# Kernel optimization log

Hardware: AMD Instinct MI355X
Metric: run time of the kernel (lower is better)

The kernel has to match this reference:

```python
import jax, jax.numpy as jnp
import numpy as np

B = 512    # batch of signals
N = 1024   # time samples per signal
M = 16384  # frequency grid points (super-resolved)


def setup_inputs() -> dict:
    key = jax.random.key(0)
    x = jax.random.normal(key, (B, 2, N), dtype=jnp.float32)  # [B, 2(re/im), N]
    xgrid = jnp.linspace(-0.5, 0.5, M, dtype=jnp.float32)      # normalized freqs
    return {"x": x, "xgrid": xgrid}


def reference(x, xgrid):
    # x: [B, 2, N] -> complex signal a + i*b
    # Periodogram at arbitrary freqs f: P(f) = |sum_n x_n * exp(-2j*pi*f*n)|^2 / N
    a = x[:, 0]  # real part [B, N]
    b = x[:, 1]  # imag part [B, N]
    Nn = x.shape[-1]
    n = jnp.arange(Nn, dtype=x.dtype)
    phase = (2.0 * jnp.pi) * xgrid[:, None] * n[None, :]  # [M, N]
    C = jnp.cos(phase)  # [M, N]
    S = jnp.sin(phase)  # [M, N]
    # x_n * (cos - i sin) = (a c + b s) + i (b c - a s)
    re = jnp.einsum('bn,mn->bm', a, C) + jnp.einsum('bn,mn->bm', b, S)
    im = jnp.einsum('bn,mn->bm', b, C) - jnp.einsum('bn,mn->bm', a, S)
    return (re * re + im * im) / Nn  # [B, M]
```

## Files before the change

kernel.cpp:

```cpp
#include <hip/hip_runtime.h>


typedef __fp16 half8  __attribute__((ext_vector_type(8)));
typedef __fp16 half2v __attribute__((ext_vector_type(2)));
typedef float  f32x4  __attribute__((ext_vector_type(4)));

#define B_SZ 512
#define N_SZ 1024
#define M_SZ 16384
#define BT 128
#define MT 128
#define KT 32

union U2 { half2v h2[2]; uint2 u; };
union BF { half2v h2[4]; half8 v; uint4 u; };

__global__ __launch_bounds__(256, 2)
void periodogram_kernel(const float* __restrict__ x, const float* __restrict__ xgrid,
                        float* __restrict__ out) {
    __shared__ __align__(16) unsigned char smem[2 * 8192];
    const int tid  = (int)threadIdx.x;
    const int lane = tid & 63;
    const int w    = tid >> 6;
    const int bid  = (int)blockIdx.x;
    const int b0 = (bid & 3) * BT;
    const int m0 = (bid >> 2) * MT;

    const int wr = (w >> 1) * 64;
    const int wc = (w & 1) * 64;

    const int row8 = tid >> 3;
    const int kk   = (tid & 7) * 4;
    const int g    = kk >> 3;
    const int kkh  = (kk >> 2) & 1;

    unsigned woff[4];
    const float* srcA[4];
#pragma unroll
    for (int rep = 0; rep < 4; ++rep) {
        const int row = row8 + rep * 32;
        const int rb = row >> 4, r16 = row & 15;
        woff[rep] = (unsigned)(rb * 1024 + ((g * 16 + (r16 ^ (g << 1))) << 4) + kkh * 8);
        srcA[rep] = x + (size_t)(b0 + row) * 2048 + kk;
    }

    half2v PC[4][4], PS[4][4];
    float c0v[4], s0v[4], C32[4], S32[4];
    const float g8f = (float)((lane >> 4) << 3);
#pragma unroll
    for (int fn = 0; fn < 4; ++fn) {
        const float xg = xgrid[m0 + wc + fn * 16 + (lane & 15)];
        float Cj[8], Sj[8];
        Cj[0] = 1.0f; Sj[0] = 0.0f;
#pragma unroll
        for (int j = 1; j < 8; ++j) {
            float p = xg * (float)j; p -= floorf(p);
            Cj[j] = __builtin_amdgcn_cosf(p);
            Sj[j] = __builtin_amdgcn_sinf(p);
        }
#pragma unroll
        for (int i = 0; i < 4; ++i) {
            PC[fn][i] = __builtin_amdgcn_cvt_pkrtz(Cj[2 * i], Cj[2 * i + 1]);
            PS[fn][i] = __builtin_amdgcn_cvt_pkrtz(Sj[2 * i], Sj[2 * i + 1]);
        }
        float p32 = xg * 32.0f; p32 -= floorf(p32);
        C32[fn] = __builtin_amdgcn_cosf(p32);
        S32[fn] = __builtin_amdgcn_sinf(p32);
        float pb = xg * g8f; pb -= floorf(pb);
        c0v[fn] = __builtin_amdgcn_cosf(pb);
        s0v[fn] = __builtin_amdgcn_sinf(pb);
    }

    f32x4 accRe[4][4], accIm[4][4];
#pragma unroll
    for (int i = 0; i < 4; ++i)
#pragma unroll
        for (int j = 0; j < 4; ++j) { accRe[i][j] = (f32x4)0.0f; accIm[i][j] = (f32x4)0.0f; }

    const unsigned roff  = (unsigned)((lane ^ ((lane >> 4) << 1)) << 4);
    const unsigned aBase = 0u    + ((unsigned)(wr >> 4) << 10) + roff;
    const unsigned bBase = 8192u + ((unsigned)(wr >> 4) << 10) + roff;

    for (int t = 0; t < N_SZ / KT; ++t) {
        const int k0 = t * KT;
        float4 va[4], vb[4];
#pragma unroll
        for (int rep = 0; rep < 4; ++rep) {
            va[rep] = *(const float4*)(srcA[rep] + k0);
            vb[rep] = *(const float4*)(srcA[rep] + k0 + 1024);
        }
        __syncthreads();
#pragma unroll
        for (int rep = 0; rep < 4; ++rep) {
            U2 pa, pb;
            pa.h2[0] = __builtin_amdgcn_cvt_pkrtz(va[rep].x, va[rep].y);
            pa.h2[1] = __builtin_amdgcn_cvt_pkrtz(va[rep].z, va[rep].w);
            pb.h2[0] = __builtin_amdgcn_cvt_pkrtz(vb[rep].x, vb[rep].y);
            pb.h2[1] = __builtin_amdgcn_cvt_pkrtz(vb[rep].z, vb[rep].w);
            *(uint2*)(smem + 0    + woff[rep]) = pa.u;
            *(uint2*)(smem + 8192 + woff[rep]) = pb.u;
        }
        __syncthreads();
        half8 fa[4], fb[4];
#pragma unroll
        for (int fm = 0; fm < 4; ++fm) {
            fa[fm] = *(const half8*)(smem + aBase + fm * 1024);
            fb[fm] = *(const half8*)(smem + bBase + fm * 1024);
        }
#pragma unroll
        for (int fn = 0; fn < 4; ++fn) {
            const float c0 = c0v[fn], s0 = s0v[fn];
            const half2v c0b = __builtin_amdgcn_cvt_pkrtz(c0, c0);
            const half2v s0b = __builtin_amdgcn_cvt_pkrtz(s0, s0);
            BF fc, fs, fns;
#pragma unroll
            for (int i = 0; i < 4; ++i) {
                fc.h2[i] = c0b * PC[fn][i] - s0b * PS[fn][i];
                fs.h2[i] = s0b * PC[fn][i] + c0b * PS[fn][i];
            }
            fns.u.x = fs.u.x ^ 0x80008000u;
            fns.u.y = fs.u.y ^ 0x80008000u;
            fns.u.z = fs.u.z ^ 0x80008000u;
            fns.u.w = fs.u.w ^ 0x80008000u;
#pragma unroll
            for (int fm = 0; fm < 4; ++fm) {
                accRe[fm][fn] = __builtin_amdgcn_mfma_f32_16x16x32_f16(fa[fm], fc.v,  accRe[fm][fn], 0, 0, 0);
                accRe[fm][fn] = __builtin_amdgcn_mfma_f32_16x16x32_f16(fb[fm], fs.v,  accRe[fm][fn], 0, 0, 0);
                accIm[fm][fn] = __builtin_amdgcn_mfma_f32_16x16x32_f16(fb[fm], fc.v,  accIm[fm][fn], 0, 0, 0);
                accIm[fm][fn] = __builtin_amdgcn_mfma_f32_16x16x32_f16(fa[fm], fns.v, accIm[fm][fn], 0, 0, 0);
            }
            c0v[fn] = __builtin_fmaf(c0, C32[fn], -(s0 * S32[fn]));
            s0v[fn] = __builtin_fmaf(s0, C32[fn],  (c0 * S32[fn]));
        }
    }

    const float inv = 1.0f / (float)N_SZ;
    const int orow0 = b0 + wr + ((lane >> 4) << 2);
    const int ocol0 = m0 + wc + (lane & 15);
#pragma unroll
    for (int fm = 0; fm < 4; ++fm)
#pragma unroll
        for (int fn = 0; fn < 4; ++fn) {
            const f32x4 r = accRe[fm][fn];
            const f32x4 im = accIm[fm][fn];
            const int col = ocol0 + fn * 16;
#pragma unroll
            for (int j = 0; j < 4; ++j) {
                const int row = orow0 + fm * 16 + j;
                out[(size_t)row * M_SZ + col] = (r[j] * r[j] + im[j] * im[j]) * inv;
            }
        }
}

extern "C" void kernel_launch(void* const* d_in, const int* in_sizes, int n_in,
                              void* d_out, int out_size, void* d_ws, size_t ws_size,
                              hipStream_t stream) {
    const float* x     = (const float*)d_in[0];
    const float* xgrid = (const float*)d_in[1];
    float* out = (float*)d_out;
    dim3 grid(B_SZ / BT * (M_SZ / MT));
    dim3 block(256);
    periodogram_kernel<<<grid, block, 0, stream>>>(x, xgrid, out);
}
```

Before: 68.93 us.

## Use Gauss three-multiply complex product to cut MFMA count per tile

Replaces the four real matrix products per complex multiply with three: a·c, b·s and (a+b)·(c−s). Real and imaginary parts are then rebuilt in the epilogue as P1+P2 and P3−P1+P2. The aim is to remove a quarter of the MFMA work. In exchange it needs a third shared-memory buffer for a+b, an extra LDS read stream, a third set of accumulators (more register pressure), and accepts some fp16 precision risk from the summed operands.

```diff
diff --git a/kernel.cpp b/kernel.cpp
--- a/kernel.cpp
+++ b/kernel.cpp
@@ -18,7 +18,7 @@
 __global__ __launch_bounds__(256, 2)
 void periodogram_kernel(const float* __restrict__ x, const float* __restrict__ xgrid,
                         float* __restrict__ out) {
-    __shared__ __align__(16) unsigned char smem[2 * 8192];
+    __shared__ __align__(16) unsigned char smem[3 * 8192];
     const int tid  = (int)threadIdx.x;
     const int lane = tid & 63;
     const int w    = tid >> 6;
@@ -71,15 +71,18 @@
         s0v[fn] = __builtin_amdgcn_sinf(pb);
     }
 
-    f32x4 accRe[4][4], accIm[4][4];
+    f32x4 accP1[4][4], accP2[4][4], accP3[4][4];
 #pragma unroll
     for (int i = 0; i < 4; ++i)
 #pragma unroll
-        for (int j = 0; j < 4; ++j) { accRe[i][j] = (f32x4)0.0f; accIm[i][j] = (f32x4)0.0f; }
+        for (int j = 0; j < 4; ++j) {
+            accP1[i][j] = (f32x4)0.0f; accP2[i][j] = (f32x4)0.0f; accP3[i][j] = (f32x4)0.0f;
+        }
 
     const unsigned roff  = (unsigned)((lane ^ ((lane >> 4) << 1)) << 4);
-    const unsigned aBase = 0u    + ((unsigned)(wr >> 4) << 10) + roff;
-    const unsigned bBase = 8192u + ((unsigned)(wr >> 4) << 10) + roff;
+    const unsigned aBase = 0u     + ((unsigned)(wr >> 4) << 10) + roff;
+    const unsigned bBase = 8192u  + ((unsigned)(wr >> 4) << 10) + roff;
+    const unsigned pBase = 16384u + ((unsigned)(wr >> 4) << 10) + roff;
 
     for (int t = 0; t < N_SZ / KT; ++t) {
         const int k0 = t * KT;
@@ -92,42 +95,42 @@
         __syncthreads();
 #pragma unroll
         for (int rep = 0; rep < 4; ++rep) {
-            U2 pa, pb;
+            U2 pa, pb, pp;
             pa.h2[0] = __builtin_amdgcn_cvt_pkrtz(va[rep].x, va[rep].y);
             pa.h2[1] = __builtin_amdgcn_cvt_pkrtz(va[rep].z, va[rep].w);
             pb.h2[0] = __builtin_amdgcn_cvt_pkrtz(vb[rep].x, vb[rep].y);
             pb.h2[1] = __builtin_amdgcn_cvt_pkrtz(vb[rep].z, vb[rep].w);
-            *(uint2*)(smem + 0    + woff[rep]) = pa.u;
-            *(uint2*)(smem + 8192 + woff[rep]) = pb.u;
+            pp.h2[0] = __builtin_amdgcn_cvt_pkrtz(va[rep].x + vb[rep].x, va[rep].y + vb[rep].y);
+            pp.h2[1] = __builtin_amdgcn_cvt_pkrtz(va[rep].z + vb[rep].z, va[rep].w + vb[rep].w);
+            *(uint2*)(smem + 0     + woff[rep]) = pa.u;
+            *(uint2*)(smem + 8192  + woff[rep]) = pb.u;
+            *(uint2*)(smem + 16384 + woff[rep]) = pp.u;
         }
         __syncthreads();
-        half8 fa[4], fb[4];
+        half8 fa[4], fb[4], fp[4];
 #pragma unroll
         for (int fm = 0; fm < 4; ++fm) {
             fa[fm] = *(const half8*)(smem + aBase + fm * 1024);
             fb[fm] = *(const half8*)(smem + bBase + fm * 1024);
+            fp[fm] = *(const half8*)(smem + pBase + fm * 1024);
         }
 #pragma unroll
         for (int fn = 0; fn < 4; ++fn) {
             const float c0 = c0v[fn], s0 = s0v[fn];
             const half2v c0b = __builtin_amdgcn_cvt_pkrtz(c0, c0);
             const half2v s0b = __builtin_amdgcn_cvt_pkrtz(s0, s0);
-            BF fc, fs, fns;
+            BF fc, fs, fd;
 #pragma unroll
             for (int i = 0; i < 4; ++i) {
                 fc.h2[i] = c0b * PC[fn][i] - s0b * PS[fn][i];
                 fs.h2[i] = s0b * PC[fn][i] + c0b * PS[fn][i];
+                fd.h2[i] = fc.h2[i] - fs.h2[i];
             }
-            fns.u.x = fs.u.x ^ 0x80008000u;
-            fns.u.y = fs.u.y ^ 0x80008000u;
-            fns.u.z = fs.u.z ^ 0x80008000u;
-            fns.u.w = fs.u.w ^ 0x80008000u;
 #pragma unroll
             for (int fm = 0; fm < 4; ++fm) {
-                accRe[fm][fn] = __builtin_amdgcn_mfma_f32_16x16x32_f16(fa[fm], fc.v,  accRe[fm][fn], 0, 0, 0);
-                accRe[fm][fn] = __builtin_amdgcn_mfma_f32_16x16x32_f16(fb[fm], fs.v,  accRe[fm][fn], 0, 0, 0);
-                accIm[fm][fn] = __builtin_amdgcn_mfma_f32_16x16x32_f16(fb[fm], fc.v,  accIm[fm][fn], 0, 0, 0);
-                accIm[fm][fn] = __builtin_amdgcn_mfma_f32_16x16x32_f16(fa[fm], fns.v, accIm[fm][fn], 0, 0, 0);
+                accP1[fm][fn] = __builtin_amdgcn_mfma_f32_16x16x32_f16(fa[fm], fc.v, accP1[fm][fn], 0, 0, 0);
+                accP2[fm][fn] = __builtin_amdgcn_mfma_f32_16x16x32_f16(fb[fm], fs.v, accP2[fm][fn], 0, 0, 0);
+                accP3[fm][fn] = __builtin_amdgcn_mfma_f32_16x16x32_f16(fp[fm], fd.v, accP3[fm][fn], 0, 0, 0);
             }
             c0v[fn] = __builtin_fmaf(c0, C32[fn], -(s0 * S32[fn]));
             s0v[fn] = __builtin_fmaf(s0, C32[fn],  (c0 * S32[fn]));
@@ -141,13 +144,16 @@
     for (int fm = 0; fm < 4; ++fm)
 #pragma unroll
         for (int fn = 0; fn < 4; ++fn) {
-            const f32x4 r = accRe[fm][fn];
-            const f32x4 im = accIm[fm][fn];
+            const f32x4 p1 = accP1[fm][fn];
+            const f32x4 p2 = accP2[fm][fn];
+            const f32x4 p3 = accP3[fm][fn];
             const int col = ocol0 + fn * 16;
 #pragma unroll
             for (int j = 0; j < 4; ++j) {
+                const float re = p1[j] + p2[j];
+                const float im = p3[j] - p1[j] + p2[j];
                 const int row = orow0 + fm * 16 + j;
-                out[(size_t)row * M_SZ + col] = (r[j] * r[j] + im[j] * im[j]) * inv;
+                out[(size_t)row * M_SZ + col] = (re * re + im * im) * inv;
             }
         }
 }
```

Measured after the change: 202.6 us. 194% more time.

## Retile to 64x256 block with K=64 and all warps sharing signal rows

Applied to the files above, without the earlier changes.

Changes the block tile from 128x128 to 64 batch rows by 256 frequencies and doubles the K step to 64, processed as two 32-wide sub-steps per barrier pair. All four waves now share the same A/B fragments and each owns a distinct 64-column frequency slice. This halves the number of sync pairs per K and cuts redundant signal loads, since the cos/sin operand is generated in registers rather than loaded. In exchange, each block does more twiddle generation per frequency column and more redundant signal loads across blocks.

```diff
diff --git a/kernel.cpp b/kernel.cpp
--- a/kernel.cpp
+++ b/kernel.cpp
@@ -8,9 +8,9 @@
 #define B_SZ 512
 #define N_SZ 1024
 #define M_SZ 16384
-#define BT 128
-#define MT 128
-#define KT 32
+#define BT 64
+#define MT 256
+#define KT 64
 
 union U2 { half2v h2[2]; uint2 u; };
 union BF { half2v h2[4]; half8 v; uint4 u; };
@@ -23,25 +23,27 @@
     const int lane = tid & 63;
     const int w    = tid >> 6;
     const int bid  = (int)blockIdx.x;
-    const int b0 = (bid & 3) * BT;
-    const int m0 = (bid >> 2) * MT;
+    const int b0 = (bid & 7) * BT;
+    const int m0 = (bid >> 3) * MT;
 
-    const int wr = (w >> 1) * 64;
-    const int wc = (w & 1) * 64;
+    const int wc = w * 64;
 
     const int row8 = tid >> 3;
     const int kk   = (tid & 7) * 4;
     const int g    = kk >> 3;
     const int kkh  = (kk >> 2) & 1;
 
-    unsigned woff[4];
-    const float* srcA[4];
+    unsigned woff[2][2];
+    const float* srcA[2];
 #pragma unroll
-    for (int rep = 0; rep < 4; ++rep) {
+    for (int rep = 0; rep < 2; ++rep) {
         const int row = row8 + rep * 32;
         const int rb = row >> 4, r16 = row & 15;
-        woff[rep] = (unsigned)(rb * 1024 + ((g * 16 + (r16 ^ (g << 1))) << 4) + kkh * 8);
         srcA[rep] = x + (size_t)(b0 + row) * 2048 + kk;
+#pragma unroll
+        for (int kh = 0; kh < 2; ++kh)
+            woff[rep][kh] = (unsigned)(rb * 2048 + kh * 1024 +
+                                       ((g * 16 + (r16 ^ (g << 1))) << 4) + kkh * 8);
     }
 
     half2v PC[4][4], PS[4][4];
@@ -77,65 +79,70 @@
 #pragma unroll
         for (int j = 0; j < 4; ++j) { accRe[i][j] = (f32x4)0.0f; accIm[i][j] = (f32x4)0.0f; }
 
-    const unsigned roff  = (unsigned)((lane ^ ((lane >> 4) << 1)) << 4);
-    const unsigned aBase = 0u    + ((unsigned)(wr >> 4) << 10) + roff;
-    const unsigned bBase = 8192u + ((unsigned)(wr >> 4) << 10) + roff;
+    const unsigned roff = (unsigned)((lane ^ ((lane >> 4) << 1)) << 4);
 
     for (int t = 0; t < N_SZ / KT; ++t) {
         const int k0 = t * KT;
-        float4 va[4], vb[4];
+        float4 va[2][2], vb[2][2];
 #pragma unroll
-        for (int rep = 0; rep < 4; ++rep) {
-            va[rep] = *(const float4*)(srcA[rep] + k0);
-            vb[rep] = *(const float4*)(srcA[rep] + k0 + 1024);
-        }
+        for (int rep = 0; rep < 2; ++rep)
+#pragma unroll
+            for (int kh = 0; kh < 2; ++kh) {
+                va[rep][kh] = *(const float4*)(srcA[rep] + k0 + kh * 32);
+                vb[rep][kh] = *(const float4*)(srcA[rep] + k0 + kh * 32 + 1024);
+            }
         __syncthreads();
 #pragma unroll
-        for (int rep = 0; rep < 4; ++rep) {
-            U2 pa, pb;
-            pa.h2[0] = __builtin_amdgcn_cvt_pkrtz(va[rep].x, va[rep].y);
-            pa.h2[1] = __builtin_amdgcn_cvt_pkrtz(va[rep].z, va[rep].w);
-            pb.h2[0] = __builtin_amdgcn_cvt_pkrtz(vb[rep].x, vb[rep].y);
-            pb.h2[1] = __builtin_amdgcn_cvt_pkrtz(vb[rep].z, vb[rep].w);
-            *(uint2*)(smem + 0    + woff[rep]) = pa.u;
-            *(uint2*)(smem + 8192 + woff[rep]) = pb.u;
-        }
+        for (int rep = 0; rep < 2; ++rep)
+#pragma unroll
+            for (int kh = 0; kh < 2; ++kh) {
+                U2 pa, pb;
+                pa.h2[0] = __builtin_amdgcn_cvt_pkrtz(va[rep][kh].x, va[rep][kh].y);
+                pa.h2[1] = __builtin_amdgcn_cvt_pkrtz(va[rep][kh].z, va[rep][kh].w);
+                pb.h2[0] = __builtin_amdgcn_cvt_pkrtz(vb[rep][kh].x, vb[rep][kh].y);
+                pb.h2[1] = __builtin_amdgcn_cvt_pkrtz(vb[rep][kh].z, vb[rep][kh].w);
+                *(uint2*)(smem + 0    + woff[rep][kh]) = pa.u;
+                *(uint2*)(smem + 8192 + woff[rep][kh]) = pb.u;
+            }
         __syncthreads();
-        half8 fa[4], fb[4];
 #pragma unroll
-        for (int fm = 0; fm < 4; ++fm) {
-            fa[fm] = *(const half8*)(smem + aBase + fm * 1024);
-            fb[fm] = *(const half8*)(smem + bBase + fm * 1024);
-        }
-#pragma unroll
-        for (int fn = 0; fn < 4; ++fn) {
-            const float c0 = c0v[fn], s0 = s0v[fn];
-            const half2v c0b = __builtin_amdgcn_cvt_pkrtz(c0, c0);
-            const half2v s0b = __builtin_amdgcn_cvt_pkrtz(s0, s0);
-            BF fc, fs, fns;
-#pragma unroll
-            for (int i = 0; i < 4; ++i) {
-                fc.h2[i] = c0b * PC[fn][i] - s0b * PS[fn][i];
-                fs.h2[i] = s0b * PC[fn][i] + c0b * PS[fn][i];
-            }
-            fns.u.x = fs.u.x ^ 0x80008000u;
-            fns.u.y = fs.u.y ^ 0x80008000u;
-            fns.u.z = fs.u.z ^ 0x80008000u;
-            fns.u.w = fs.u.w ^ 0x80008000u;
+        for (int s = 0; s < 2; ++s) {
+            half8 fa[4], fb[4];
 #pragma unroll
             for (int fm = 0; fm < 4; ++fm) {
-                accRe[fm][fn] = __builtin_amdgcn_mfma_f32_16x16x32_f16(fa[fm], fc.v,  accRe[fm][fn], 0, 0, 0);
-                accRe[fm][fn] = __builtin_amdgcn_mfma_f32_16x16x32_f16(fb[fm], fs.v,  accRe[fm][fn], 0, 0, 0);
-                accIm[fm][fn] = __builtin_amdgcn_mfma_f32_16x16x32_f16(fb[fm], fc.v,  accIm[fm][fn], 0, 0, 0);
-                accIm[fm][fn] = __builtin_amdgcn_mfma_f32_16x16x32_f16(fa[fm], fns.v, accIm[fm][fn], 0, 0, 0);
+                fa[fm] = *(const half8*)(smem + (unsigned)(fm * 2048 + s * 1024) + roff);
+                fb[fm] = *(const half8*)(smem + 8192u + (unsigned)(fm * 2048 + s * 1024) + roff);
             }
-            c0v[fn] = __builtin_fmaf(c0, C32[fn], -(s0 * S32[fn]));
-            s0v[fn] = __builtin_fmaf(s0, C32[fn],  (c0 * S32[fn]));
+#pragma unroll
+            for (int fn = 0; fn < 4; ++fn) {
+                const float c0 = c0v[fn], s0 = s0v[fn];
+                const half2v c0b = __builtin_amdgcn_cvt_pkrtz(c0, c0);
+                const half2v s0b = __builtin_amdgcn_cvt_pkrtz(s0, s0);
+                BF fc, fs, fns;
+#pragma unroll
+                for (int i = 0; i < 4; ++i) {
+                    fc.h2[i] = c0b * PC[fn][i] - s0b * PS[fn][i];
+                    fs.h2[i] = s0b * PC[fn][i] + c0b * PS[fn][i];
+                }
+                fns.u.x = fs.u.x ^ 0x80008000u;
+                fns.u.y = fs.u.y ^ 0x80008000u;
+                fns.u.z = fs.u.z ^ 0x80008000u;
+                fns.u.w = fs.u.w ^ 0x80008000u;
+#pragma unroll
+                for (int fm = 0; fm < 4; ++fm) {
+                    accRe[fm][fn] = __builtin_amdgcn_mfma_f32_16x16x32_f16(fa[fm], fc.v,  accRe[fm][fn], 0, 0, 0);
+                    accRe[fm][fn] = __builtin_amdgcn_mfma_f32_16x16x32_f16(fb[fm], fs.v,  accRe[fm][fn], 0, 0, 0);
+                    accIm[fm][fn] = __builtin_amdgcn_mfma_f32_16x16x32_f16(fb[fm], fc.v,  accIm[fm][fn], 0, 0, 0);
+                    accIm[fm][fn] = __builtin_amdgcn_mfma_f32_16x16x32_f16(fa[fm], fns.v, accIm[fm][fn], 0, 0, 0);
+                }
+                c0v[fn] = __builtin_fmaf(c0, C32[fn], -(s0 * S32[fn]));
+                s0v[fn] = __builtin_fmaf(s0, C32[fn],  (c0 * S32[fn]));
+            }
         }
     }
 
     const float inv = 1.0f / (float)N_SZ;
-    const int orow0 = b0 + wr + ((lane >> 4) << 2);
+    const int orow0 = b0 + ((lane >> 4) << 2);
     const int ocol0 = m0 + wc + (lane & 15);
 #pragma unroll
     for (int fm = 0; fm < 4; ++fm)
@@ -158,7 +165,7 @@
     const float* x     = (const float*)d_in[0];
     const float* xgrid = (const float*)d_in[1];
     float* out = (float*)d_out;
-    dim3 grid(B_SZ / BT * (M_SZ / MT));
+    dim3 grid(8 * (M_SZ / MT));
     dim3 block(256);
     periodogram_kernel<<<grid, block, 0, stream>>>(x, xgrid, out);
 }
```

New measurement: 97.94 us. +42.1%, slower.

## Pre-convert input to fp16 MFMA fragment layout in workspace, drop LDS staging

Applied to the files above, without the earlier changes.

Adds a separate conversion kernel that turns the fp32 signal into fp16 and writes it to workspace already arranged in the MFMA fragment order. The main kernel then loads its A/B fragments straight from global memory with one 16-byte load per fragment. This removes the per-tile LDS stores, both __syncthreads barriers and the repeated fp32-to-fp16 conversions. The costs are an extra kernel launch, workspace traffic, and global-load latency inside the MFMA loop with no software prefetch. Each block also loses the data sharing it had through LDS, though L2 should serve the repeated reads.

```diff
diff --git a/kernel.cpp b/kernel.cpp
--- a/kernel.cpp
+++ b/kernel.cpp
@@ -11,14 +11,36 @@
 #define BT 128
 #define MT 128
 #define KT 32
+#define WS_ARR 1048576
 
-union U2 { half2v h2[2]; uint2 u; };
+union U4 { half2v h2[4]; uint4 u; };
 union BF { half2v h2[4]; half8 v; uint4 u; };
 
+__global__ __launch_bounds__(256)
+void cvt_kernel(const float* __restrict__ x, unsigned char* __restrict__ ws) {
+    const int id  = (int)blockIdx.x * 256 + (int)threadIdx.x;
+    const int arr = id >> 16;
+    const int rem = id & 65535;
+    const int rb  = rem >> 11;
+    const int kc  = (rem >> 6) & 31;
+    const int l6  = rem & 63;
+    const int r16 = l6 >> 2;
+    const int g   = l6 & 3;
+    const float* src = x + (size_t)(rb * 16 + r16) * 2048 + arr * 1024 + kc * 32 + g * 8;
+    const float4 v0 = *(const float4*)src;
+    const float4 v1 = *(const float4*)(src + 4);
+    U4 u;
+    u.h2[0] = __builtin_amdgcn_cvt_pkrtz(v0.x, v0.y);
+    u.h2[1] = __builtin_amdgcn_cvt_pkrtz(v0.z, v0.w);
+    u.h2[2] = __builtin_amdgcn_cvt_pkrtz(v1.x, v1.y);
+    u.h2[3] = __builtin_amdgcn_cvt_pkrtz(v1.z, v1.w);
+    *(uint4*)(ws + (size_t)arr * WS_ARR + (size_t)(rb * 32 + kc) * 1024 + (g * 16 + r16) * 16) = u.u;
+}
+
 __global__ __launch_bounds__(256, 2)
-void periodogram_kernel(const float* __restrict__ x, const float* __restrict__ xgrid,
+void periodogram_kernel(const unsigned char* __restrict__ ws,
+                        const float* __restrict__ xgrid,
                         float* __restrict__ out) {
-    __shared__ __align__(16) unsigned char smem[2 * 8192];
     const int tid  = (int)threadIdx.x;
     const int lane = tid & 63;
     const int w    = tid >> 6;
@@ -29,19 +51,13 @@
     const int wr = (w >> 1) * 64;
     const int wc = (w & 1) * 64;
 
-    const int row8 = tid >> 3;
-    const int kk   = (tid & 7) * 4;
-    const int g    = kk >> 3;
-    const int kkh  = (kk >> 2) & 1;
-
-    unsigned woff[4];
-    const float* srcA[4];
+    const unsigned char* pA[4];
+    const unsigned char* pB[4];
 #pragma unroll
-    for (int rep = 0; rep < 4; ++rep) {
-        const int row = row8 + rep * 32;
-        const int rb = row >> 4, r16 = row & 15;
-        woff[rep] = (unsigned)(rb * 1024 + ((g * 16 + (r16 ^ (g << 1))) << 4) + kkh * 8);
-        srcA[rep] = x + (size_t)(b0 + row) * 2048 + kk;
+    for (int fm = 0; fm < 4; ++fm) {
+        const int rb = ((b0 + wr) >> 4) + fm;
+        pA[fm] = ws + (size_t)(rb * 32) * 1024 + (size_t)(lane * 16);
+        pB[fm] = pA[fm] + WS_ARR;
     }
 
     half2v PC[4][4], PS[4][4];
@@ -77,35 +93,13 @@
 #pragma unroll
         for (int j = 0; j < 4; ++j) { accRe[i][j] = (f32x4)0.0f; accIm[i][j] = (f32x4)0.0f; }
 
-    const unsigned roff  = (unsigned)((lane ^ ((lane >> 4) << 1)) << 4);
-    const unsigned aBase = 0u    + ((unsigned)(wr >> 4) << 10) + roff;
-    const unsigned bBase = 8192u + ((unsigned)(wr >> 4) << 10) + roff;
-
     for (int t = 0; t < N_SZ / KT; ++t) {
-        const int k0 = t * KT;
-        float4 va[4], vb[4];
-#pragma unroll
-        for (int rep = 0; rep < 4; ++rep) {
-            va[rep] = *(const float4*)(srcA[rep] + k0);
-            vb[rep] = *(const float4*)(srcA[rep] + k0 + 1024);
-        }
-        __syncthreads();
-#pragma unroll
-        for (int rep = 0; rep < 4; ++rep) {
-            U2 pa, pb;
-            pa.h2[0] = __builtin_amdgcn_cvt_pkrtz(va[rep].x, va[rep].y);
-            pa.h2[1] = __builtin_amdgcn_cvt_pkrtz(va[rep].z, va[rep].w);
-            pb.h2[0] = __builtin_amdgcn_cvt_pkrtz(vb[rep].x, vb[rep].y);
-            pb.h2[1] = __builtin_amdgcn_cvt_pkrtz(vb[rep].z, vb[rep].w);
-            *(uint2*)(smem + 0    + woff[rep]) = pa.u;
-            *(uint2*)(smem + 8192 + woff[rep]) = pb.u;
-        }
-        __syncthreads();
         half8 fa[4], fb[4];
+        const unsigned off = (unsigned)(t * 1024);
 #pragma unroll
         for (int fm = 0; fm < 4; ++fm) {
-            fa[fm] = *(const half8*)(smem + aBase + fm * 1024);
-            fb[fm] = *(const half8*)(smem + bBase + fm * 1024);
+            fa[fm] = *(const half8*)(pA[fm] + off);
+            fb[fm] = *(const half8*)(pB[fm] + off);
         }
 #pragma unroll
         for (int fn = 0; fn < 4; ++fn) {
@@ -158,7 +152,9 @@
     const float* x     = (const float*)d_in[0];
     const float* xgrid = (const float*)d_in[1];
     float* out = (float*)d_out;
+    unsigned char* ws = (unsigned char*)d_ws;
+    cvt_kernel<<<512, 256, 0, stream>>>(x, ws);
     dim3 grid(B_SZ / BT * (M_SZ / MT));
     dim3 block(256);
-    periodogram_kernel<<<grid, block, 0, stream>>>(x, xgrid, out);
+    periodogram_kernel<<<grid, block, 0, stream>>>(ws, xgrid, out);
 }
```

New measurement: 65.37 us. -5.2%, faster.
